# Kernel optimization log

Measured on AMD Instinct MI355X. Metric: run time of the kernel, lower is better.

## Reference

```python
import jax, jax.numpy as jnp
import numpy as np

F_HEAD_THR, B_TAIL_THR = 0.5, 0.5

# big_w index map: 0 f_W_h, 1 b_W_t, 2 f_W_r, 3 f_W_g, 4 f_W_x, 5 b_W_r, 6 b_W_g, 7 b_W_x, 8 f_Wx2, 9 b_Wx2
# fc_w index map:  0 f_start_head, 1 f_end_head, 2 f_start_tail, 3 f_end_tail,
#                  4 b_start_tail, 5 b_end_tail, 6 b_start_head, 7 b_end_head, 8 V


def extract_first_embeddings(token_embs, start_probs, end_probs, thr):
    """Extract the first detected span per batch element, zero-padded to L."""
    B, L, H = token_embs.shape
    pos = jnp.arange(L)
    smask = start_probs > thr                      # (B, L)
    emask = end_probs > thr
    has_s = smask.any(axis=1)
    s_idx = jnp.argmax(smask, axis=1)              # first start (0 if none)
    ecand = emask & (pos[None, :] >= s_idx[:, None])
    has_e = ecand.any(axis=1)
    e_idx = jnp.where(has_e, jnp.argmax(ecand, axis=1), s_idx)
    span_len = e_idx - s_idx + 1
    gidx = jnp.clip(s_idx[:, None] + pos[None, :], 0, L - 1)   # (B, L)
    mask = (pos[None, :] < span_len[:, None]) & has_s[:, None]
    padded = jnp.take_along_axis(token_embs, gidx[:, :, None], axis=1)
    padded = padded * mask[:, :, None].astype(token_embs.dtype)
    return padded, mask.astype(token_embs.dtype), s_idx


def _attention_context(proj_r, proj_g, proj_x, v_w, v_b, token_embs):
    # e = tanh(W_r r + W_g g + W_x x) broadcast to (B, L, R, H); score via V
    e = jnp.tanh(proj_x[:, :, None, :] + proj_g[:, None, None, :] + proj_r[None, None, :, :])
    v = jnp.einsum('blrh,h->blr', e, v_w) + v_b        # (B, L, R)
    A = jax.nn.softmax(v, axis=1)                      # softmax over L
    C = jnp.einsum('blr,blh->brh', A, token_embs)      # (B, R, H)
    return C


def _span_logits(Hik, C, token_embs, w, b):
    # Hijk[b,l,r] = Hik[b,l] + C[b,r] + token[b,l]; linear head decomposes:
    return ((Hik + token_embs) @ w)[:, :, None] + (C @ w)[:, None, :] + b


def reference(h_gs, token_embs, f_rel_embs, b_rel_transe, r_proj_w, r_proj_b, fc_w, fc_b, big_w, big_b):
    b_rel_embs = b_rel_transe @ r_proj_w + r_proj_b    # (R, H)

    # span-boundary heads on raw token embeddings
    f_hs = token_embs @ fc_w[0] + fc_b[0]              # (B, L)
    f_he = token_embs @ fc_w[1] + fc_b[1]
    b_ts = token_embs @ fc_w[4] + fc_b[4]
    b_te = token_embs @ fc_w[5] + fc_b[5]

    f_pad, f_mask, _ = extract_first_embeddings(token_embs, jax.nn.sigmoid(f_hs), jax.nn.sigmoid(f_he), F_HEAD_THR)
    b_pad, b_mask, _ = extract_first_embeddings(token_embs, jax.nn.sigmoid(b_ts), jax.nn.sigmoid(b_te), B_TAIL_THR)

    f_h_w = (f_pad @ big_w[0] + big_b[0]) * f_mask[:, :, None]
    b_t_w = (b_pad @ big_w[1] + big_b[1]) * b_mask[:, :, None]

    # small projections computed once, broadcast inside attention
    f_C = _attention_context(f_rel_embs @ big_w[2] + big_b[2],
                             h_gs @ big_w[3] + big_b[3],
                             token_embs @ big_w[4] + big_b[4],
                             fc_w[8], fc_b[8], token_embs)
    b_C = _attention_context(b_rel_embs @ big_w[5] + big_b[5],
                             h_gs @ big_w[6] + big_b[6],
                             token_embs @ big_w[7] + big_b[7],
                             fc_w[8], fc_b[8], token_embs)

    f_Hik = f_h_w + token_embs @ big_w[8] + big_b[8]
    b_Hik = b_t_w + token_embs @ big_w[9] + big_b[9]

    f_tail_s = _span_logits(f_Hik, f_C, token_embs, fc_w[2], fc_b[2])
    f_tail_e = _span_logits(f_Hik, f_C, token_embs, fc_w[3], fc_b[3])
    b_head_s = _span_logits(b_Hik, b_C, token_embs, fc_w[6], fc_b[6])
    b_head_e = _span_logits(b_Hik, b_C, token_embs, fc_w[7], fc_b[7])

    return (f_hs[..., None], f_he[..., None], f_tail_s, f_tail_e,
            b_ts[..., None], b_te[..., None], b_head_s, b_head_e)


def setup_inputs() -> dict:
    B, L, R, H, D = 4, 128, 48, 768, 100
    key = jax.random.key(0)
    ks = jax.random.split(key, 10)
    sc = 0.05
    return {
        'h_gs': jax.random.normal(ks[0], (B, H), jnp.float32),
        'token_embs': jax.random.normal(ks[1], (B, L, H), jnp.float32),
        'f_rel_embs': jax.random.normal(ks[2], (R, H), jnp.float32),
        'b_rel_transe': jax.random.normal(ks[3], (R, D), jnp.float32),
        'r_proj_w': jax.random.normal(ks[4], (D, H), jnp.float32) * sc,
        'r_proj_b': jnp.zeros((H,), jnp.float32),
        'fc_w': jax.random.normal(ks[5], (9, H), jnp.float32) * sc,
        'fc_b': jnp.zeros((9,), jnp.float32),
        'big_w': jax.random.normal(ks[6], (10, H, H), jnp.float32) * sc,
        'big_b': jnp.zeros((10, H), jnp.float32),
    }
```

## Files before the change

kernel.cpp:

```cpp
#include <hip/hip_runtime.h>
#include <hip/hip_bf16.h>

constexpr int H = 768, B = 4, L = 128, R = 48, D = 100;
constexpr int BL = B * L;
constexpr int P_SZ = BL * H;

constexpr int OUT_FHS = 0, OUT_FHE = 512, OUT_FTS = 1024, OUT_FTE = 25600,
              OUT_BTS = 50176, OUT_BTE = 50688, OUT_BHS = 51200, OUT_BHE = 75776;

constexpr int WS_BREL = 6 * P_SZ;
constexpr int WS_PRF  = WS_BREL + R * H;
constexpr int WS_PRB  = WS_PRF + R * H;
constexpr int WS_PGF  = WS_PRB + R * H;
constexpr int WS_PGB  = WS_PGF + B * H;
constexpr int WS_VF   = WS_PGB + B * H;
constexpr int WS_VB   = WS_VF + B * R * L;
constexpr int WS_T2   = WS_VB + B * R * L;
constexpr int WS_U    = WS_T2 + 4 * BL;
constexpr int WS_CC   = WS_U + 4 * BL;
constexpr int WS_SPAN = WS_CC + 4 * B * R;
constexpr int WS_BF16 = WS_SPAN + 16;

constexpr int UB_TOK  = 0;
constexpr int UB_FREL = UB_TOK + BL * H;
constexpr int UB_BREL = UB_FREL + R * H;
constexpr int UB_HGS  = UB_BREL + R * H;
constexpr int UB_WT   = UB_HGS + B * H;

typedef __attribute__((ext_vector_type(8))) short short8;
typedef __attribute__((ext_vector_type(4))) float floatx4;

__device__ __forceinline__ float tanh_fast(float x) {
    float u = __builtin_amdgcn_exp2f(x * 2.8853900817779268f);
    return 1.0f - 2.0f * __builtin_amdgcn_rcpf(1.0f + u);
}

__device__ __forceinline__ float wave_sum(float v) {
    #pragma unroll
    for (int off = 32; off; off >>= 1) v += __shfl_down(v, off);
    return v;
}

__device__ __forceinline__ ushort f2bf(float x) {
    __hip_bfloat16 h = __float2bfloat16(x);
    return __builtin_bit_cast(ushort, h);
}

__device__ __forceinline__ ushort4 f2bf4(float4 v) {
    ushort4 u;
    u.x = f2bf(v.x); u.y = f2bf(v.y); u.z = f2bf(v.z); u.w = f2bf(v.w);
    return u;
}

__global__ __launch_bounds__(256) void k_setup(const float* __restrict__ tok,
                                               const float* __restrict__ h_gs,
                                               const float* __restrict__ f_rel,
                                               const float* __restrict__ b_rt,
                                               const float* __restrict__ rpw,
                                               const float* __restrict__ rpb,
                                               const float* __restrict__ fcw,
                                               const float* __restrict__ fcb,
                                               const float* __restrict__ bigw,
                                               float* __restrict__ out,
                                               float* __restrict__ ws) {
    __shared__ float lds[64 * 65];
    ushort* ub = (ushort*)(ws + WS_BF16);
    int blk = blockIdx.x, tid = threadIdx.x;

    if (blk < 128) {
        int wid = blk * 4 + (tid >> 6), lane = tid & 63;
        int b = wid >> 7, l = wid & 127;
        const float* tr = tok + (b * L + l) * H;
        float p0 = 0, p1 = 0, p2 = 0, p3 = 0, p4 = 0, p5 = 0, p6 = 0, p7 = 0;
        #pragma unroll
        for (int j = 0; j < H / 64; ++j) {
            int h = lane + j * 64;
            float t = tr[h];
            p0 += t * fcw[h];
            p1 += t * fcw[H + h];
            p4 += t * fcw[4 * H + h];
            p5 += t * fcw[5 * H + h];
            p2 += t * fcw[2 * H + h];
            p3 += t * fcw[3 * H + h];
            p6 += t * fcw[6 * H + h];
            p7 += t * fcw[7 * H + h];
        }
        p0 = wave_sum(p0); p1 = wave_sum(p1); p4 = wave_sum(p4); p5 = wave_sum(p5);
        p2 = wave_sum(p2); p3 = wave_sum(p3); p6 = wave_sum(p6); p7 = wave_sum(p7);
        if (lane == 0) {
            int idx = b * L + l;
            out[OUT_FHS + idx] = p0 + fcb[0];
            out[OUT_FHE + idx] = p1 + fcb[1];
            out[OUT_BTS + idx] = p4 + fcb[4];
            out[OUT_BTE + idx] = p5 + fcb[5];
            float* t2 = ws + WS_T2;
            t2[idx] = p2; t2[BL + idx] = p3; t2[2 * BL + idx] = p6; t2[3 * BL + idx] = p7;
        }
    } else if (blk < 176) {
        int r = blk - 128;
        if (tid < D) lds[tid] = b_rt[r * D + tid];
        __syncthreads();
        #pragma unroll
        for (int jj = 0; jj < 3; ++jj) {
            int h = tid + jj * 256;
            float acc = rpb[h];
            for (int k = 0; k < D; ++k) acc += lds[k] * rpw[k * H + h];
            ws[WS_BREL + r * H + h] = acc;
            ub[UB_BREL + r * H + h] = f2bf(acc);
        }
    } else if (blk < 200) {
        int base = (blk - 176) * 16384;
        #pragma unroll
        for (int i = 0; i < 16; ++i) {
            int e = base + i * 1024 + tid * 4;
            float4 v = *(const float4*)&tok[e];
            *(ushort4*)&ub[UB_TOK + e] = f2bf4(v);
        }
    } else if (blk < 204) {
        int base = (blk - 200) * 9216;
        #pragma unroll
        for (int i = 0; i < 9; ++i) {
            int e = base + i * 1024 + tid * 4;
            float4 v = *(const float4*)&f_rel[e];
            *(ushort4*)&ub[UB_FREL + e] = f2bf4(v);
        }
    } else if (blk == 204) {
        #pragma unroll
        for (int i = 0; i < 3; ++i) {
            int e = i * 1024 + tid * 4;
            float4 v = *(const float4*)&h_gs[e];
            *(ushort4*)&ub[UB_HGS + e] = f2bf4(v);
        }
    } else {
        int wb = blk - 205;
        int j = wb / 144, t = wb - j * 144;
        int kt = t / 12, nt = t - kt * 12;
        int k0 = kt * 64, n0 = nt * 64;
        const float* W = bigw + (size_t)j * H * H;
        ushort* WT = ub + UB_WT + (size_t)j * H * H;
        #pragma unroll
        for (int it = 0; it < 4; ++it) {
            int kk = (tid >> 4) + it * 16;
            int nn = (tid & 15) * 4;
            float4 v = *(const float4*)&W[(k0 + kk) * H + n0 + nn];
            lds[kk * 65 + nn + 0] = v.x;
            lds[kk * 65 + nn + 1] = v.y;
            lds[kk * 65 + nn + 2] = v.z;
            lds[kk * 65 + nn + 3] = v.w;
        }
        __syncthreads();
        #pragma unroll
        for (int it = 0; it < 4; ++it) {
            int nn = (tid >> 4) + it * 16;
            int kk = (tid & 15) * 4;
            float4 v;
            v.x = lds[(kk + 0) * 65 + nn];
            v.y = lds[(kk + 1) * 65 + nn];
            v.z = lds[(kk + 2) * 65 + nn];
            v.w = lds[(kk + 3) * 65 + nn];
            *(ushort4*)&WT[(n0 + nn) * H + k0 + kk] = f2bf4(v);
        }
    }
}

__global__ void k_span(const float* __restrict__ out, float* __restrict__ ws) {
    int w = threadIdx.x >> 6, lane = threadIdx.x & 63;
    int ctx = w >> 2, b = w & 3;
    const float* sp = out + (ctx ? OUT_BTS : OUT_FHS) + b * L;
    const float* ep = out + (ctx ? OUT_BTE : OUT_FHE) + b * L;
    unsigned long long s0 = __ballot(sp[lane] > 0.f);
    unsigned long long s1 = __ballot(sp[lane + 64] > 0.f);
    unsigned long long e0 = __ballot(ep[lane] > 0.f);
    unsigned long long e1 = __ballot(ep[lane + 64] > 0.f);
    if (lane == 0) {
        int s, len;
        if (s0 == 0 && s1 == 0) { s = 0; len = 0; }
        else {
            s = s0 ? __builtin_ctzll(s0) : 64 + __builtin_ctzll(s1);
            int e;
            if (s < 64) {
                unsigned long long m0 = (e0 >> s) << s;
                e = m0 ? __builtin_ctzll(m0) : (e1 ? 64 + __builtin_ctzll(e1) : s);
            } else {
                int s2 = s - 64;
                unsigned long long m1 = (e1 >> s2) << s2;
                e = m1 ? 64 + __builtin_ctzll(m1) : s;
            }
            len = e - s + 1;
        }
        int* span = (int*)(ws + WS_SPAN);
        span[ctx * 8 + b] = s;
        span[ctx * 8 + 4 + b] = len;
    }
}

struct MfmaDesc { const ushort* A; const ushort* W; const float* bias; float* O; int M; };
struct MfmaArgs { MfmaDesc d[10]; int off[11]; };

__global__ __launch_bounds__(64) void k_mfma(MfmaArgs args) {
    int blk = blockIdx.x;
    int p = 0;
    while (p < 9 && blk >= args.off[p + 1]) ++p;
    MfmaDesc dd = args.d[p];
    int t = blk - args.off[p];
    int mt = t / 12, nt = t - mt * 12;
    int m0 = mt * 32, n0 = nt * 64;
    int lane = threadIdx.x;
    int lr = lane & 15, q = lane >> 4;
    int Mm1 = dd.M - 1;
    int r0 = min(m0 + lr, Mm1);
    int r1 = min(m0 + 16 + lr, Mm1);
    const ushort* a0p = dd.A + r0 * H + q * 8;
    const ushort* a1p = dd.A + r1 * H + q * 8;
    const ushort* bp  = dd.W + (n0 + lr) * H + q * 8;
    floatx4 acc[2][4] = {};
    #pragma unroll
    for (int k0 = 0; k0 < H; k0 += 32) {
        short8 a0 = *(const short8*)(a0p + k0);
        short8 a1 = *(const short8*)(a1p + k0);
        #pragma unroll
        for (int j = 0; j < 4; ++j) {
            short8 bf = *(const short8*)(bp + j * 16 * H + k0);
            acc[0][j] = __builtin_amdgcn_mfma_f32_16x16x32_bf16(a0, bf, acc[0][j], 0, 0, 0);
            acc[1][j] = __builtin_amdgcn_mfma_f32_16x16x32_bf16(a1, bf, acc[1][j], 0, 0, 0);
        }
    }
    #pragma unroll
    for (int j = 0; j < 4; ++j) {
        int col = n0 + j * 16 + lr;
        float bv = dd.bias[col];
        #pragma unroll
        for (int i = 0; i < 2; ++i) {
            int rowb = m0 + i * 16 + q * 4;
            #pragma unroll
            for (int r = 0; r < 4; ++r) {
                int row = rowb + r;
                if (row < dd.M) dd.O[row * H + col] = acc[i][j][r] + bv;
            }
        }
    }
}

__global__ __launch_bounds__(256) void k_attn_v(float* __restrict__ ws,
                                                const float* __restrict__ fcw,
                                                const float* __restrict__ fcb) {
    int ctx = blockIdx.y;
    int bl = blockIdx.x;
    int b = bl >> 7;
    const float* px = ws + (ctx ? 3 : 2) * P_SZ + bl * H;
    const float* pg = ws + (ctx ? WS_PGB : WS_PGF) + b * H;
    const float* pr = ws + (ctx ? WS_PRB : WS_PRF);
    float* vout = ws + (ctx ? WS_VB : WS_VF);
    __shared__ float s_x[H];
    __shared__ float s_vw[H];
    for (int idx = threadIdx.x; idx < H; idx += 256) {
        s_x[idx] = px[idx] + pg[idx];
        s_vw[idx] = fcw[8 * H + idx];
    }
    __syncthreads();
    int w = threadIdx.x >> 6, lane = threadIdx.x & 63;
    int l = bl & 127;
    float vb = fcb[8];
    for (int r = w; r < R; r += 4) {
        const float* prr = pr + r * H;
        float p = 0.f;
        #pragma unroll
        for (int j = 0; j < H / 64; ++j) {
            int h = lane + j * 64;
            p += tanh_fast(s_x[h] + prr[h]) * s_vw[h];
        }
        p = wave_sum(p);
        if (lane == 0) vout[(b * R + r) * L + l] = p + vb;
    }
}

__global__ __launch_bounds__(64) void k_attn2(float* __restrict__ ws) {
    int row = blockIdx.x;
    int lane = threadIdx.x;
    int ctx = row >= 192 ? 1 : 0;
    int rr = row - ctx * 192;
    int b = rr / R;
    const float* base = ws + (ctx ? WS_VB : WS_VF) + rr * L;
    float x0 = base[lane], x1 = base[lane + 64];
    float m = fmaxf(x0, x1);
    #pragma unroll
    for (int off = 32; off; off >>= 1) m = fmaxf(m, __shfl_xor(m, off));
    constexpr float LOG2E = 1.4426950408889634f;
    float e0 = __builtin_amdgcn_exp2f((x0 - m) * LOG2E);
    float e1 = __builtin_amdgcn_exp2f((x1 - m) * LOG2E);
    float s = e0 + e1;
    #pragma unroll
    for (int off = 32; off; off >>= 1) s += __shfl_xor(s, off);
    float inv = __builtin_amdgcn_rcpf(s);
    const float* tA = ws + WS_T2 + (ctx * 2 + 0) * BL + b * L;
    const float* tB = ws + WS_T2 + (ctx * 2 + 1) * BL + b * L;
    float pa = e0 * tA[lane] + e1 * tA[lane + 64];
    float pb = e0 * tB[lane] + e1 * tB[lane + 64];
    pa = wave_sum(pa); pb = wave_sum(pb);
    if (lane == 0) {
        float* c = ws + WS_CC;
        c[(ctx * 2 + 0) * 192 + rr] = pa * inv;
        c[(ctx * 2 + 1) * 192 + rr] = pb * inv;
    }
}

__global__ __launch_bounds__(256) void k_udots(const float* __restrict__ tok,
                                               const float* __restrict__ fcw,
                                               float* __restrict__ ws) {
    int wid = blockIdx.x * 4 + (threadIdx.x >> 6);
    int lane = threadIdx.x & 63;
    int b = wid >> 7, l = wid & 127;
    const int* span = (const int*)(ws + WS_SPAN);
    int fs = span[b], flen = span[4 + b];
    int bs = span[8 + b], blen = span[12 + b];
    bool fm = l < flen, bm = l < blen;
    float fmf = fm ? 1.f : 0.f, bmf = bm ? 1.f : 0.f;
    const float* tr = tok + (b * L + l) * H;
    const float* p4r = ws + 4 * P_SZ + (b * L + l) * H;
    const float* p5r = ws + 5 * P_SZ + (b * L + l) * H;
    const float* g0r = ws + 0 * P_SZ + (b * L + (fm ? fs + l : 0)) * H;
    const float* g1r = ws + 1 * P_SZ + (b * L + (bm ? bs + l : 0)) * H;
    float pf2 = 0, pf3 = 0, pb6 = 0, pb7 = 0;
    #pragma unroll
    for (int j = 0; j < H / 64; ++j) {
        int h = lane + j * 64;
        float t = tr[h];
        float sf = t + p4r[h] + fmf * g0r[h];
        float sb = t + p5r[h] + bmf * g1r[h];
        pf2 += sf * fcw[2 * H + h];
        pf3 += sf * fcw[3 * H + h];
        pb6 += sb * fcw[6 * H + h];
        pb7 += sb * fcw[7 * H + h];
    }
    pf2 = wave_sum(pf2); pf3 = wave_sum(pf3);
    pb6 = wave_sum(pb6); pb7 = wave_sum(pb7);
    if (lane == 0) {
        int idx = b * L + l;
        float* u = ws + WS_U;
        u[idx] = pf2; u[BL + idx] = pf3; u[2 * BL + idx] = pb6; u[3 * BL + idx] = pb7;
    }
}

__global__ __launch_bounds__(256) void k_bcast(const float* __restrict__ fcb,
                                               const float* __restrict__ ws,
                                               float* __restrict__ out) {
    int t = blockIdx.x * 256 + threadIdx.x;
    int head = t / 24576;
    int rem = t - head * 24576;
    int b = rem / 6144;
    int lr = rem - b * 6144;
    int l = lr / 48;
    int r = lr - l * 48;
    const int out_off[4] = {OUT_FTS, OUT_FTE, OUT_BHS, OUT_BHE};
    const int wb[4] = {2, 3, 6, 7};
    const float* u = ws + WS_U;
    const float* c = ws + WS_CC;
    out[out_off[head] + rem] = u[head * BL + b * L + l] + c[head * 192 + b * R + r] + fcb[wb[head]];
}

extern "C" void kernel_launch(void* const* d_in, const int* in_sizes, int n_in,
                              void* d_out, int out_size, void* d_ws, size_t ws_size,
                              hipStream_t stream) {
    const float* h_gs  = (const float*)d_in[0];
    const float* tok   = (const float*)d_in[1];
    const float* f_rel = (const float*)d_in[2];
    const float* b_rt  = (const float*)d_in[3];
    const float* rpw   = (const float*)d_in[4];
    const float* rpb   = (const float*)d_in[5];
    const float* fcw   = (const float*)d_in[6];
    const float* fcb   = (const float*)d_in[7];
    const float* bigw  = (const float*)d_in[8];
    const float* bigb  = (const float*)d_in[9];
    float* out = (float*)d_out;
    float* ws  = (float*)d_ws;
    const ushort* ub = (const ushort*)(ws + WS_BF16);

    k_setup<<<1645, 256, 0, stream>>>(tok, h_gs, f_rel, b_rt, rpw, rpb, fcw, fcb, bigw, out, ws);
    k_span<<<1, 512, 0, stream>>>(out, ws);

    MfmaArgs ma;
    const int wj[6] = {0, 1, 4, 7, 8, 9};
    for (int j = 0; j < 6; ++j)
        ma.d[j] = MfmaDesc{ub + UB_TOK, ub + UB_WT + (size_t)wj[j] * H * H,
                           bigb + wj[j] * H, ws + (size_t)j * P_SZ, BL};
    ma.d[6] = MfmaDesc{ub + UB_FREL, ub + UB_WT + 2 * (size_t)H * H, bigb + 2 * H, ws + WS_PRF, R};
    ma.d[7] = MfmaDesc{ub + UB_BREL, ub + UB_WT + 5 * (size_t)H * H, bigb + 5 * H, ws + WS_PRB, R};
    ma.d[8] = MfmaDesc{ub + UB_HGS,  ub + UB_WT + 3 * (size_t)H * H, bigb + 3 * H, ws + WS_PGF, B};
    ma.d[9] = MfmaDesc{ub + UB_HGS,  ub + UB_WT + 6 * (size_t)H * H, bigb + 6 * H, ws + WS_PGB, B};
    int off = 0;
    for (int p = 0; p < 10; ++p) {
        ma.off[p] = off;
        int mtiles = (ma.d[p].M + 31) / 32;
        off += mtiles * 12;
    }
    ma.off[10] = off;
    k_mfma<<<off, 64, 0, stream>>>(ma);

    k_attn_v<<<dim3(512, 2), 256, 0, stream>>>(ws, fcw, fcb);
    k_attn2<<<384, 64, 0, stream>>>(ws);
    k_udots<<<128, 256, 0, stream>>>(tok, fcw, ws);
    k_bcast<<<384, 256, 0, stream>>>(fcb, ws, out);
}
```

Baseline: 150.2 us.

## Fuse epilogue kernels, fold span into GEMM, retile MFMA with LDS staging

The span-detection kernel is folded into an extra block of the MFMA launch. The GEMM moves from one-wave 32x64 tiles to four-wave 64x64 tiles that stage A and B through padded LDS. The attention-score kernel now handles four token positions per block, keeping x in registers and reusing each relation row across them. The softmax-context, per-token dot and broadcast kernels are merged into one k_epi kernel, and an unused fp32 b_rel store is dropped. Together these cut the launch count and intermediate traffic, but k_epi runs only 32 blocks, which may leave most of the GPU idle in that stage.

Result: no change. 152.3 us (+1.4%).

```diff
diff --git a/kernel.cpp b/kernel.cpp
--- a/kernel.cpp
+++ b/kernel.cpp
@@ -105,7 +105,6 @@
             int h = tid + jj * 256;
             float acc = rpb[h];
             for (int k = 0; k < D; ++k) acc += lds[k] * rpw[k * H + h];
-            ws[WS_BREL + r * H + h] = acc;
             ub[UB_BREL + r * H + h] = f2bf(acc);
         }
     } else if (blk < 200) {
@@ -163,79 +162,101 @@
     }
 }
 
-__global__ void k_span(const float* __restrict__ out, float* __restrict__ ws) {
-    int w = threadIdx.x >> 6, lane = threadIdx.x & 63;
-    int ctx = w >> 2, b = w & 3;
-    const float* sp = out + (ctx ? OUT_BTS : OUT_FHS) + b * L;
-    const float* ep = out + (ctx ? OUT_BTE : OUT_FHE) + b * L;
-    unsigned long long s0 = __ballot(sp[lane] > 0.f);
-    unsigned long long s1 = __ballot(sp[lane + 64] > 0.f);
-    unsigned long long e0 = __ballot(ep[lane] > 0.f);
-    unsigned long long e1 = __ballot(ep[lane + 64] > 0.f);
-    if (lane == 0) {
-        int s, len;
-        if (s0 == 0 && s1 == 0) { s = 0; len = 0; }
-        else {
-            s = s0 ? __builtin_ctzll(s0) : 64 + __builtin_ctzll(s1);
-            int e;
-            if (s < 64) {
-                unsigned long long m0 = (e0 >> s) << s;
-                e = m0 ? __builtin_ctzll(m0) : (e1 ? 64 + __builtin_ctzll(e1) : s);
-            } else {
-                int s2 = s - 64;
-                unsigned long long m1 = (e1 >> s2) << s2;
-                e = m1 ? 64 + __builtin_ctzll(m1) : s;
-            }
-            len = e - s + 1;
-        }
-        int* span = (int*)(ws + WS_SPAN);
-        span[ctx * 8 + b] = s;
-        span[ctx * 8 + 4 + b] = len;
-    }
-}
-
 struct MfmaDesc { const ushort* A; const ushort* W; const float* bias; float* O; int M; };
 struct MfmaArgs { MfmaDesc d[10]; int off[11]; };
 
-__global__ __launch_bounds__(64) void k_mfma(MfmaArgs args) {
-    int blk = blockIdx.x;
+constexpr int AST = 72;
+
+__global__ __launch_bounds__(256) void k_mfma(MfmaArgs args, const float* __restrict__ out,
+                                              float* __restrict__ ws) {
+    int blk = blockIdx.x, tid = threadIdx.x;
+    int lane = tid & 63, w = tid >> 6;
+
+    if (blk == 624) {
+        for (int pp = w; pp < 8; pp += 4) {
+            int ctx = pp >> 2, b = pp & 3;
+            const float* sp = out + (ctx ? OUT_BTS : OUT_FHS) + b * L;
+            const float* ep = out + (ctx ? OUT_BTE : OUT_FHE) + b * L;
+            unsigned long long s0 = __ballot(sp[lane] > 0.f);
+            unsigned long long s1 = __ballot(sp[lane + 64] > 0.f);
+            unsigned long long e0 = __ballot(ep[lane] > 0.f);
+            unsigned long long e1 = __ballot(ep[lane + 64] > 0.f);
+            if (lane == 0) {
+                int s, len;
+                if (s0 == 0 && s1 == 0) { s = 0; len = 0; }
+                else {
+                    s = s0 ? __builtin_ctzll(s0) : 64 + __builtin_ctzll(s1);
+                    int e;
+                    if (s < 64) {
+                        unsigned long long m0 = (e0 >> s) << s;
+                        e = m0 ? __builtin_ctzll(m0) : (e1 ? 64 + __builtin_ctzll(e1) : s);
+                    } else {
+                        int s2 = s - 64;
+                        unsigned long long m1 = (e1 >> s2) << s2;
+                        e = m1 ? 64 + __builtin_ctzll(m1) : s;
+                    }
+                    len = e - s + 1;
+                }
+                int* span = (int*)(ws + WS_SPAN);
+                span[ctx * 8 + b] = s;
+                span[ctx * 8 + 4 + b] = len;
+            }
+        }
+        return;
+    }
+
     int p = 0;
     while (p < 9 && blk >= args.off[p + 1]) ++p;
     MfmaDesc dd = args.d[p];
     int t = blk - args.off[p];
     int mt = t / 12, nt = t - mt * 12;
-    int m0 = mt * 32, n0 = nt * 64;
-    int lane = threadIdx.x;
+    int m0 = mt * 64, n0 = nt * 64;
+
+    __shared__ __align__(16) ushort As[64 * AST];
+    __shared__ __align__(16) ushort Bs[64 * AST];
+
+    int seg = tid & 7;
+    int row2 = tid >> 3;
+    int Mm1 = dd.M - 1;
+
+    int wm = w >> 1, wn = w & 1;
     int lr = lane & 15, q = lane >> 4;
-    int Mm1 = dd.M - 1;
-    int r0 = min(m0 + lr, Mm1);
-    int r1 = min(m0 + 16 + lr, Mm1);
-    const ushort* a0p = dd.A + r0 * H + q * 8;
-    const ushort* a1p = dd.A + r1 * H + q * 8;
-    const ushort* bp  = dd.W + (n0 + lr) * H + q * 8;
-    floatx4 acc[2][4] = {};
+    floatx4 acc[2][2] = {};
+
+    for (int k0 = 0; k0 < H; k0 += 64) {
+        #pragma unroll
+        for (int it = 0; it < 2; ++it) {
+            int r = row2 + it * 32;
+            int ar = min(m0 + r, Mm1);
+            *(short8*)&As[r * AST + seg * 8] = *(const short8*)&dd.A[ar * H + k0 + seg * 8];
+            *(short8*)&Bs[r * AST + seg * 8] = *(const short8*)&dd.W[(n0 + r) * H + k0 + seg * 8];
+        }
+        __syncthreads();
+        #pragma unroll
+        for (int ks = 0; ks < 64; ks += 32) {
+            short8 a0 = *(const short8*)&As[(wm * 32 + lr) * AST + ks + q * 8];
+            short8 a1 = *(const short8*)&As[(wm * 32 + 16 + lr) * AST + ks + q * 8];
+            short8 b0 = *(const short8*)&Bs[(wn * 32 + lr) * AST + ks + q * 8];
+            short8 b1 = *(const short8*)&Bs[(wn * 32 + 16 + lr) * AST + ks + q * 8];
+            acc[0][0] = __builtin_amdgcn_mfma_f32_16x16x32_bf16(a0, b0, acc[0][0], 0, 0, 0);
+            acc[0][1] = __builtin_amdgcn_mfma_f32_16x16x32_bf16(a0, b1, acc[0][1], 0, 0, 0);
+            acc[1][0] = __builtin_amdgcn_mfma_f32_16x16x32_bf16(a1, b0, acc[1][0], 0, 0, 0);
+            acc[1][1] = __builtin_amdgcn_mfma_f32_16x16x32_bf16(a1, b1, acc[1][1], 0, 0, 0);
+        }
+        __syncthreads();
+    }
+
     #pragma unroll
-    for (int k0 = 0; k0 < H; k0 += 32) {
-        short8 a0 = *(const short8*)(a0p + k0);
-        short8 a1 = *(const short8*)(a1p + k0);
-        #pragma unroll
-        for (int j = 0; j < 4; ++j) {
-            short8 bf = *(const short8*)(bp + j * 16 * H + k0);
-            acc[0][j] = __builtin_amdgcn_mfma_f32_16x16x32_bf16(a0, bf, acc[0][j], 0, 0, 0);
-            acc[1][j] = __builtin_amdgcn_mfma_f32_16x16x32_bf16(a1, bf, acc[1][j], 0, 0, 0);
-        }
-    }
-    #pragma unroll
-    for (int j = 0; j < 4; ++j) {
-        int col = n0 + j * 16 + lr;
+    for (int j = 0; j < 2; ++j) {
+        int col = n0 + wn * 32 + j * 16 + lr;
         float bv = dd.bias[col];
         #pragma unroll
         for (int i = 0; i < 2; ++i) {
-            int rowb = m0 + i * 16 + q * 4;
+            int rowb = m0 + wm * 32 + i * 16 + q * 4;
             #pragma unroll
-            for (int r = 0; r < 4; ++r) {
-                int row = rowb + r;
-                if (row < dd.M) dd.O[row * H + col] = acc[i][j][r] + bv;
+            for (int rr = 0; rr < 4; ++rr) {
+                int row = rowb + rr;
+                if (row < dd.M) dd.O[row * H + col] = acc[i][j][rr] + bv;
             }
         }
     }
@@ -245,117 +266,122 @@
                                                 const float* __restrict__ fcw,
                                                 const float* __restrict__ fcb) {
     int ctx = blockIdx.y;
-    int bl = blockIdx.x;
-    int b = bl >> 7;
-    const float* px = ws + (ctx ? 3 : 2) * P_SZ + bl * H;
+    int b = blockIdx.x >> 5;
+    int l0 = (blockIdx.x & 31) * 4;
+    int lane = threadIdx.x & 63, w = threadIdx.x >> 6;
+
+    const float* pxb = ws + (ctx ? 3 : 2) * P_SZ + (b * L + l0) * H;
     const float* pg = ws + (ctx ? WS_PGB : WS_PGF) + b * H;
     const float* pr = ws + (ctx ? WS_PRB : WS_PRF);
-    float* vout = ws + (ctx ? WS_VB : WS_VF);
-    __shared__ float s_x[H];
-    __shared__ float s_vw[H];
-    for (int idx = threadIdx.x; idx < H; idx += 256) {
-        s_x[idx] = px[idx] + pg[idx];
-        s_vw[idx] = fcw[8 * H + idx];
-    }
-    __syncthreads();
-    int w = threadIdx.x >> 6, lane = threadIdx.x & 63;
-    int l = bl & 127;
+    float* vout = ws + (ctx ? WS_VB : WS_VF) + b * R * L + l0;
+
+    float x[4][12], vw[12];
+    #pragma unroll
+    for (int j = 0; j < 12; ++j) {
+        int h = lane + j * 64;
+        float g = pg[h];
+        vw[j] = fcw[8 * H + h];
+        #pragma unroll
+        for (int ll = 0; ll < 4; ++ll) x[ll][j] = pxb[ll * H + h] + g;
+    }
     float vb = fcb[8];
+
     for (int r = w; r < R; r += 4) {
         const float* prr = pr + r * H;
-        float p = 0.f;
-        #pragma unroll
-        for (int j = 0; j < H / 64; ++j) {
-            int h = lane + j * 64;
-            p += tanh_fast(s_x[h] + prr[h]) * s_vw[h];
-        }
-        p = wave_sum(p);
-        if (lane == 0) vout[(b * R + r) * L + l] = p + vb;
-    }
-}
-
-__global__ __launch_bounds__(64) void k_attn2(float* __restrict__ ws) {
-    int row = blockIdx.x;
-    int lane = threadIdx.x;
-    int ctx = row >= 192 ? 1 : 0;
-    int rr = row - ctx * 192;
-    int b = rr / R;
-    const float* base = ws + (ctx ? WS_VB : WS_VF) + rr * L;
-    float x0 = base[lane], x1 = base[lane + 64];
-    float m = fmaxf(x0, x1);
-    #pragma unroll
-    for (int off = 32; off; off >>= 1) m = fmaxf(m, __shfl_xor(m, off));
-    constexpr float LOG2E = 1.4426950408889634f;
-    float e0 = __builtin_amdgcn_exp2f((x0 - m) * LOG2E);
-    float e1 = __builtin_amdgcn_exp2f((x1 - m) * LOG2E);
-    float s = e0 + e1;
-    #pragma unroll
-    for (int off = 32; off; off >>= 1) s += __shfl_xor(s, off);
-    float inv = __builtin_amdgcn_rcpf(s);
+        float pv[12];
+        #pragma unroll
+        for (int j = 0; j < 12; ++j) pv[j] = prr[lane + j * 64];
+        float p[4] = {0.f, 0.f, 0.f, 0.f};
+        #pragma unroll
+        for (int j = 0; j < 12; ++j) {
+            float pvj = pv[j], vwj = vw[j];
+            #pragma unroll
+            for (int ll = 0; ll < 4; ++ll)
+                p[ll] += tanh_fast(x[ll][j] + pvj) * vwj;
+        }
+        #pragma unroll
+        for (int ll = 0; ll < 4; ++ll) p[ll] = wave_sum(p[ll]);
+        if (lane == 0) {
+            #pragma unroll
+            for (int ll = 0; ll < 4; ++ll) vout[r * L + ll] = p[ll] + vb;
+        }
+    }
+}
+
+__global__ __launch_bounds__(256) void k_epi(const float* __restrict__ tok,
+                                             const float* __restrict__ fcw,
+                                             const float* __restrict__ fcb,
+                                             float* __restrict__ ws,
+                                             float* __restrict__ out) {
+    int ctx = blockIdx.z, b = blockIdx.y, l0 = blockIdx.x * 32;
+    int lane = threadIdx.x & 63, w = threadIdx.x >> 6;
+    __shared__ float c2[2][R];
+    __shared__ float uu[2][32];
+
+    const float* vbase = ws + (ctx ? WS_VB : WS_VF) + b * R * L;
     const float* tA = ws + WS_T2 + (ctx * 2 + 0) * BL + b * L;
     const float* tB = ws + WS_T2 + (ctx * 2 + 1) * BL + b * L;
-    float pa = e0 * tA[lane] + e1 * tA[lane + 64];
-    float pb = e0 * tB[lane] + e1 * tB[lane + 64];
-    pa = wave_sum(pa); pb = wave_sum(pb);
-    if (lane == 0) {
-        float* c = ws + WS_CC;
-        c[(ctx * 2 + 0) * 192 + rr] = pa * inv;
-        c[(ctx * 2 + 1) * 192 + rr] = pb * inv;
-    }
-}
-
-__global__ __launch_bounds__(256) void k_udots(const float* __restrict__ tok,
-                                               const float* __restrict__ fcw,
-                                               float* __restrict__ ws) {
-    int wid = blockIdx.x * 4 + (threadIdx.x >> 6);
-    int lane = threadIdx.x & 63;
-    int b = wid >> 7, l = wid & 127;
+    for (int r = w; r < R; r += 4) {
+        const float* vr = vbase + r * L;
+        float x0 = vr[lane], x1 = vr[lane + 64];
+        float m = fmaxf(x0, x1);
+        #pragma unroll
+        for (int off = 32; off; off >>= 1) m = fmaxf(m, __shfl_xor(m, off));
+        constexpr float LOG2E = 1.4426950408889634f;
+        float e0 = __builtin_amdgcn_exp2f((x0 - m) * LOG2E);
+        float e1 = __builtin_amdgcn_exp2f((x1 - m) * LOG2E);
+        float s = e0 + e1;
+        float pa = e0 * tA[lane] + e1 * tA[lane + 64];
+        float pb = e0 * tB[lane] + e1 * tB[lane + 64];
+        #pragma unroll
+        for (int off = 32; off; off >>= 1) {
+            s += __shfl_xor(s, off);
+            pa += __shfl_xor(pa, off);
+            pb += __shfl_xor(pb, off);
+        }
+        if (lane == 0) {
+            float inv = __builtin_amdgcn_rcpf(s);
+            c2[0][r] = pa * inv;
+            c2[1][r] = pb * inv;
+        }
+    }
+
     const int* span = (const int*)(ws + WS_SPAN);
-    int fs = span[b], flen = span[4 + b];
-    int bs = span[8 + b], blen = span[12 + b];
-    bool fm = l < flen, bm = l < blen;
-    float fmf = fm ? 1.f : 0.f, bmf = bm ? 1.f : 0.f;
-    const float* tr = tok + (b * L + l) * H;
-    const float* p4r = ws + 4 * P_SZ + (b * L + l) * H;
-    const float* p5r = ws + 5 * P_SZ + (b * L + l) * H;
-    const float* g0r = ws + 0 * P_SZ + (b * L + (fm ? fs + l : 0)) * H;
-    const float* g1r = ws + 1 * P_SZ + (b * L + (bm ? bs + l : 0)) * H;
-    float pf2 = 0, pf3 = 0, pb6 = 0, pb7 = 0;
+    int s0 = span[ctx * 8 + b], sl = span[ctx * 8 + 4 + b];
+    const float* wA = fcw + (ctx ? 6 : 2) * H;
+    const float* wB = fcw + (ctx ? 7 : 3) * H;
+    const float* pX = ws + (ctx ? 5 : 4) * (size_t)P_SZ;
+    const float* pG = ws + (ctx ? 1 : 0) * (size_t)P_SZ;
     #pragma unroll
-    for (int j = 0; j < H / 64; ++j) {
-        int h = lane + j * 64;
-        float t = tr[h];
-        float sf = t + p4r[h] + fmf * g0r[h];
-        float sb = t + p5r[h] + bmf * g1r[h];
-        pf2 += sf * fcw[2 * H + h];
-        pf3 += sf * fcw[3 * H + h];
-        pb6 += sb * fcw[6 * H + h];
-        pb7 += sb * fcw[7 * H + h];
-    }
-    pf2 = wave_sum(pf2); pf3 = wave_sum(pf3);
-    pb6 = wave_sum(pb6); pb7 = wave_sum(pb7);
-    if (lane == 0) {
-        int idx = b * L + l;
-        float* u = ws + WS_U;
-        u[idx] = pf2; u[BL + idx] = pf3; u[2 * BL + idx] = pb6; u[3 * BL + idx] = pb7;
-    }
-}
-
-__global__ __launch_bounds__(256) void k_bcast(const float* __restrict__ fcb,
-                                               const float* __restrict__ ws,
-                                               float* __restrict__ out) {
-    int t = blockIdx.x * 256 + threadIdx.x;
-    int head = t / 24576;
-    int rem = t - head * 24576;
-    int b = rem / 6144;
-    int lr = rem - b * 6144;
-    int l = lr / 48;
-    int r = lr - l * 48;
-    const int out_off[4] = {OUT_FTS, OUT_FTE, OUT_BHS, OUT_BHE};
-    const int wb[4] = {2, 3, 6, 7};
-    const float* u = ws + WS_U;
-    const float* c = ws + WS_CC;
-    out[out_off[head] + rem] = u[head * BL + b * L + l] + c[head * 192 + b * R + r] + fcb[wb[head]];
+    for (int i = 0; i < 8; ++i) {
+        int l_loc = w * 8 + i, l = l0 + l_loc;
+        bool msk = l < sl;
+        float mf = msk ? 1.f : 0.f;
+        const float* tr = tok + (b * L + l) * H;
+        const float* xr = pX + (b * L + l) * H;
+        const float* gr = pG + (b * L + (msk ? s0 + l : 0)) * H;
+        float pf = 0.f, pg2 = 0.f;
+        #pragma unroll
+        for (int j = 0; j < 12; ++j) {
+            int h = lane + j * 64;
+            float sv = tr[h] + xr[h] + mf * gr[h];
+            pf += sv * wA[h];
+            pg2 += sv * wB[h];
+        }
+        pf = wave_sum(pf); pg2 = wave_sum(pg2);
+        if (lane == 0) { uu[0][l_loc] = pf; uu[1][l_loc] = pg2; }
+    }
+    __syncthreads();
+
+    const int out_off4[4] = {OUT_FTS, OUT_FTE, OUT_BHS, OUT_BHE};
+    float bias0 = fcb[ctx ? 6 : 2], bias1 = fcb[ctx ? 7 : 3];
+    int o0 = out_off4[ctx * 2 + 0], o1 = out_off4[ctx * 2 + 1];
+    for (int idx = threadIdx.x; idx < 32 * R; idx += 256) {
+        int l_loc = idx / R, r = idx - l_loc * R;
+        int o = b * (L * R) + (l0 + l_loc) * R + r;
+        out[o0 + o] = uu[0][l_loc] + c2[0][r] + bias0;
+        out[o1 + o] = uu[1][l_loc] + c2[1][r] + bias1;
+    }
 }
 
 extern "C" void kernel_launch(void* const* d_in, const int* in_sizes, int n_in,
@@ -376,7 +402,6 @@
     const ushort* ub = (const ushort*)(ws + WS_BF16);
 
     k_setup<<<1645, 256, 0, stream>>>(tok, h_gs, f_rel, b_rt, rpw, rpb, fcw, fcb, bigw, out, ws);
-    k_span<<<1, 512, 0, stream>>>(out, ws);
 
     MfmaArgs ma;
     const int wj[6] = {0, 1, 4, 7, 8, 9};
@@ -390,14 +415,12 @@
     int off = 0;
     for (int p = 0; p < 10; ++p) {
         ma.off[p] = off;
-        int mtiles = (ma.d[p].M + 31) / 32;
+        int mtiles = (ma.d[p].M + 63) / 64;
         off += mtiles * 12;
     }
     ma.off[10] = off;
-    k_mfma<<<off, 64, 0, stream>>>(ma);
-
-    k_attn_v<<<dim3(512, 2), 256, 0, stream>>>(ws, fcw, fcb);
-    k_attn2<<<384, 64, 0, stream>>>(ws);
-    k_udots<<<128, 256, 0, stream>>>(tok, fcw, ws);
-    k_bcast<<<384, 256, 0, stream>>>(fcb, ws, out);
-}
+    k_mfma<<<off + 1, 256, 0, stream>>>(ma, out, ws);
+
+    k_attn_v<<<dim3(128, 2), 256, 0, stream>>>(ws, fcw, fcb);
+    k_epi<<<dim3(4, 4, 2), 256, 0, stream>>>(tok, fcw, fcb, ws, out);
+}
```
